# Optimization experiments

Measured on AMD Instinct MI355X. Metric: run time of the kernel, lower is better.

The kernel has to match this reference:

```python
import jax, jax.numpy as jnp
import numpy as np

N = 100_000       # nodes
E = 600_000       # edges
D_IN = 128
D_OUT = 128


def setup_inputs() -> dict:
    key = jax.random.key(0)
    k0, k1, k2, k3, k4, k5 = jax.random.split(key, 6)
    node_feature = jax.random.normal(k0, (N, D_IN), dtype=jnp.float32)
    edge_index = jax.random.randint(k1, (2, E), 0, N, dtype=jnp.int32)
    s = 1.0 / np.sqrt(D_IN)  # torch nn.Linear default init range
    W1 = jax.random.uniform(k2, (D_OUT, D_IN), jnp.float32, -s, s)
    b1 = jax.random.uniform(k3, (D_OUT,), jnp.float32, -s, s)
    W2 = jax.random.uniform(k4, (D_OUT, D_IN), jnp.float32, -s, s)
    b2 = jax.random.uniform(k5, (D_OUT,), jnp.float32, -s, s)
    return {"node_feature": node_feature, "edge_index": edge_index,
            "W1": W1, "b1": b1, "W2": W2, "b2": b2}


def reference(node_feature, edge_index, W1, b1, W2, b2):
    # h1 = lin1(x)
    h1 = node_feature @ W1.T + b1                       # [N, D_OUT]
    src, dst = edge_index[0], edge_index[1]
    # scatter(x[src], dst, reduce='mul', dim_size=N): segment product,
    # identity 1 for nodes with no incoming edges
    msgs = node_feature[src]                            # [E, D_IN]
    aggr = jax.ops.segment_prod(msgs, dst, num_segments=N)  # [N, D_IN]
    h2 = aggr @ W2.T + b2                               # [N, D_OUT]
    return h1 * h2
```

## Files before the change

### kernel.cpp

```cpp
#include <hip/hip_runtime.h>

#define NN 100000
#define NE 600000
#define D  128
#define CAP 64
#define NT (NN / 16)

typedef __attribute__((ext_vector_type(8))) short short8;
typedef __attribute__((ext_vector_type(4))) float floatx4;

__device__ __forceinline__ unsigned short f2bf(float f) {
    union { float f; unsigned int u; } a; a.f = f;
    unsigned int r = a.u + 0x7fff + ((a.u >> 16) & 1);
    return (unsigned short)(r >> 16);
}
__device__ __forceinline__ float bf2f(unsigned short h) {
    union { unsigned int u; float f; } a; a.u = ((unsigned int)h) << 16;
    return a.f;
}

__global__ __launch_bounds__(256) void prep_kernel(const float* __restrict__ W1,
                                                   const float* __restrict__ W2,
                                                   short8* __restrict__ wfrag,
                                                   int* __restrict__ counts) {
    int idx = blockIdx.x * 256 + threadIdx.x;
    for (int j = idx; j < NN; j += 4096) counts[j] = 0;

    int m2 = idx >> 11;
    int rem = idx & 2047;
    int c = rem >> 8;
    int q = (rem >> 6) & 3;
    int l = rem & 63;
    const float* W = m2 ? W2 : W1;
    int row = c * 16 + (l & 15);
    int kb = q * 32 + 8 * (l >> 4);
    const float* src = &W[row * D + kb];
    short8 h, lo;
#pragma unroll
    for (int j = 0; j < 8; ++j) {
        float v = src[j];
        unsigned short hh = f2bf(v);
        h[j]  = (short)hh;
        lo[j] = (short)f2bf(v - bf2f(hh));
    }
    wfrag[(((m2 * 2 + 0) * 8 + c) * 4 + q) * 64 + l] = h;
    wfrag[(((m2 * 2 + 1) * 8 + c) * 4 + q) * 64 + l] = lo;
}


__global__ void bucket_kernel(const int* __restrict__ src, const int* __restrict__ dst,
                              int* __restrict__ counts, int* __restrict__ bucket, int e) {
    int i = blockIdx.x * blockDim.x + threadIdx.x;
    if (i < e) {
        int d = dst[i];
        int pos = atomicAdd(&counts[d], 1);
        if (pos < CAP) bucket[(size_t)d * CAP + pos] = src[i];
    }
}

__global__ __launch_bounds__(512, 1)
void fused_kernel(const float* __restrict__ x,
                  const int* __restrict__ counts,
                  const int* __restrict__ bucket,
                  const short8* __restrict__ wfrag,
                  const float* __restrict__ b1,
                  const float* __restrict__ b2,
                  float* __restrict__ out) {
    __shared__ short8 sW[2 * 8 * 4 * 64];

    const int lane = threadIdx.x & 63;
    const int wv   = threadIdx.x >> 6;
    const int r16  = lane & 15;
    const int g    = lane >> 4;

    const int tile = blockIdx.x * 8 + wv;
    const bool live = (tile < NT);
    const int base = tile * 16;
    const size_t rowoff = live ? ((size_t)(base + r16) * D + g * 8) : 0;

    short8 st[8];
#pragma unroll
    for (int k = 0; k < 8; ++k) st[k] = wfrag[threadIdx.x + k * 512];

    floatx4 p[8];
#pragma unroll
    for (int k = 0; k < 8; ++k) p[k] = (floatx4)1.f;
    if (live) {
        const int node = base + r16;
        int cnt = counts[node]; if (cnt > CAP) cnt = CAP;
        const int* bp = &bucket[(size_t)node * CAP];
        int i = 0;
        for (; i + 2 <= cnt; i += 2) {
            int s0 = bp[i], s1 = bp[i + 1];
            const float* xr0 = &x[(size_t)s0 * D + g * 8];
            const float* xr1 = &x[(size_t)s1 * D + g * 8];
#pragma unroll
            for (int q = 0; q < 4; ++q) {
                floatx4 a0 = *(const floatx4*)&xr0[q * 32];
                floatx4 a1 = *(const floatx4*)&xr0[q * 32 + 4];
                floatx4 c0 = *(const floatx4*)&xr1[q * 32];
                floatx4 c1 = *(const floatx4*)&xr1[q * 32 + 4];
                p[2 * q]     *= a0 * c0;
                p[2 * q + 1] *= a1 * c1;
            }
        }
        if (i < cnt) {
            int s0 = bp[i];
            const float* xr0 = &x[(size_t)s0 * D + g * 8];
#pragma unroll
            for (int q = 0; q < 4; ++q) {
                p[2 * q]     *= *(const floatx4*)&xr0[q * 32];
                p[2 * q + 1] *= *(const floatx4*)&xr0[q * 32 + 4];
            }
        }
    }
    short8 gh[4], gl[4];
#pragma unroll
    for (int q = 0; q < 4; ++q) {
        short8 h, l;
#pragma unroll
        for (int jj = 0; jj < 4; ++jj) {
            unsigned short hh = f2bf(p[2 * q][jj]);
            h[jj] = (short)hh;
            l[jj] = (short)f2bf(p[2 * q][jj] - bf2f(hh));
            unsigned short hh2 = f2bf(p[2 * q + 1][jj]);
            h[4 + jj] = (short)hh2;
            l[4 + jj] = (short)f2bf(p[2 * q + 1][jj] - bf2f(hh2));
        }
        gh[q] = h; gl[q] = l;
    }

#pragma unroll
    for (int k = 0; k < 8; ++k) sW[threadIdx.x + k * 512] = st[k];
    __syncthreads();

    floatx4 acc[8];
#pragma unroll
    for (int c = 0; c < 8; ++c) acc[c] = (floatx4)0.f;

    floatx4 h1[8];
    if (live) {
        const float* xr = &x[rowoff];
#pragma unroll
        for (int q = 0; q < 4; ++q) {
            floatx4 v0 = *(const floatx4*)&xr[q * 32];
            floatx4 v1 = *(const floatx4*)&xr[q * 32 + 4];
            short8 fh, fl;
#pragma unroll
            for (int jj = 0; jj < 4; ++jj) {
                unsigned short hh = f2bf(v0[jj]);
                fh[jj] = (short)hh;
                fl[jj] = (short)f2bf(v0[jj] - bf2f(hh));
                unsigned short hh2 = f2bf(v1[jj]);
                fh[4 + jj] = (short)hh2;
                fl[4 + jj] = (short)f2bf(v1[jj] - bf2f(hh2));
            }
#pragma unroll
            for (int c = 0; c < 8; ++c) {
                short8 bh = sW[((0 * 8 + c) * 4 + q) * 64 + lane];
                short8 bl = sW[((1 * 8 + c) * 4 + q) * 64 + lane];
                acc[c] = __builtin_amdgcn_mfma_f32_16x16x32_bf16(fh, bh, acc[c], 0, 0, 0);
                acc[c] = __builtin_amdgcn_mfma_f32_16x16x32_bf16(fl, bh, acc[c], 0, 0, 0);
                acc[c] = __builtin_amdgcn_mfma_f32_16x16x32_bf16(fh, bl, acc[c], 0, 0, 0);
            }
        }
#pragma unroll
        for (int c = 0; c < 8; ++c) {
            float bb = b1[c * 16 + r16];
            floatx4 t = acc[c];
            t[0] += bb; t[1] += bb; t[2] += bb; t[3] += bb;
            h1[c] = t;
            acc[c] = (floatx4)0.f;
        }
    }

    __syncthreads();
    for (int i = threadIdx.x; i < 4096; i += 512) sW[i] = wfrag[4096 + i];
    __syncthreads();

    if (live) {
#pragma unroll
        for (int q = 0; q < 4; ++q) {
#pragma unroll
            for (int c = 0; c < 8; ++c) {
                short8 bh = sW[((0 * 8 + c) * 4 + q) * 64 + lane];
                short8 bl = sW[((1 * 8 + c) * 4 + q) * 64 + lane];
                acc[c] = __builtin_amdgcn_mfma_f32_16x16x32_bf16(gh[q], bh, acc[c], 0, 0, 0);
                acc[c] = __builtin_amdgcn_mfma_f32_16x16x32_bf16(gl[q], bh, acc[c], 0, 0, 0);
                acc[c] = __builtin_amdgcn_mfma_f32_16x16x32_bf16(gh[q], bl, acc[c], 0, 0, 0);
            }
        }
#pragma unroll
        for (int c = 0; c < 8; ++c) {
            float bb = b2[c * 16 + r16];
#pragma unroll
            for (int r = 0; r < 4; ++r) {
                out[(size_t)(base + g * 4 + r) * D + c * 16 + r16] =
                    h1[c][r] * (acc[c][r] + bb);
            }
        }
    }
}


extern "C" void kernel_launch(void* const* d_in, const int* in_sizes, int n_in,
                              void* d_out, int out_size, void* d_ws, size_t ws_size,
                              hipStream_t stream) {
    const float* x  = (const float*)d_in[0];
    const int*   ei = (const int*)d_in[1];
    const float* W1 = (const float*)d_in[2];
    const float* b1 = (const float*)d_in[3];
    const float* W2 = (const float*)d_in[4];
    const float* b2 = (const float*)d_in[5];
    float* out = (float*)d_out;

    const int n = NN, e = NE;
    const int* src = ei;
    const int* dst = ei + e;

    char* ws = (char*)d_ws;
    short8* wfrag = (short8*)ws;                ws += 8192 * 16;
    int* counts = (int*)ws;                     ws += (size_t)n * sizeof(int);
    ws += 256 - ((uintptr_t)ws & 255);
    int* bucket = (int*)ws;

    prep_kernel<<<16, 256, 0, stream>>>(W1, W2, wfrag, counts);
    bucket_kernel<<<(e + 255) / 256, 256, 0, stream>>>(src, dst, counts, bucket, e);
    fused_kernel<<<(NT + 7) / 8, 512, 0, stream>>>(x, counts, bucket, wfrag, b1, b2, out);
}
```

Before: 131.8 us.

## Sort nodes by in-degree so each wave gathers for similar-degree rows

Adds a degree histogram, a scan and a counting-sort permutation of nodes by clamped in-degree. The fused kernel then processes tiles of permuted nodes and scatters output rows through the permutation. This balances per-lane gather loop trip counts within a wave, reducing divergence from the max-degree lane. It adds three small kernels plus a memset, and makes x row reads and output writes non-contiguous.

```diff
diff --git a/kernel.cpp b/kernel.cpp
--- a/kernel.cpp
+++ b/kernel.cpp
@@ -21,11 +21,8 @@
 
 __global__ __launch_bounds__(256) void prep_kernel(const float* __restrict__ W1,
                                                    const float* __restrict__ W2,
-                                                   short8* __restrict__ wfrag,
-                                                   int* __restrict__ counts) {
+                                                   short8* __restrict__ wfrag) {
     int idx = blockIdx.x * 256 + threadIdx.x;
-    for (int j = idx; j < NN; j += 4096) counts[j] = 0;
-
     int m2 = idx >> 11;
     int rem = idx & 2047;
     int c = rem >> 8;
@@ -58,10 +55,59 @@
     }
 }
 
+
+__global__ __launch_bounds__(256) void dhist_kernel(const int* __restrict__ counts,
+                                                    int* __restrict__ dhist, int n) {
+    __shared__ int lh[CAP + 1];
+    int t = threadIdx.x;
+    if (t <= CAP) lh[t] = 0;
+    __syncthreads();
+    int i = blockIdx.x * 256 + t;
+    if (i < n) {
+        int d = counts[i]; if (d > CAP) d = CAP;
+        atomicAdd(&lh[d], 1);
+    }
+    __syncthreads();
+    if (t <= CAP && lh[t]) atomicAdd(&dhist[t], lh[t]);
+}
+
+
+__global__ __launch_bounds__(64) void dscan_kernel(const int* __restrict__ dhist,
+                                                   int* __restrict__ dcur) {
+    if (threadIdx.x == 0) {
+        int run = 0;
+        for (int d = 0; d <= CAP; ++d) { dcur[d] = run; run += dhist[d]; }
+    }
+}
+
+
+__global__ __launch_bounds__(256) void perm_kernel(const int* __restrict__ counts,
+                                                   int* __restrict__ dcur,
+                                                   int* __restrict__ perm, int n) {
+    __shared__ int lh[CAP + 1], lbase[CAP + 1], lcur[CAP + 1];
+    int t = threadIdx.x;
+    if (t <= CAP) { lh[t] = 0; lcur[t] = 0; }
+    __syncthreads();
+    int i = blockIdx.x * 256 + t;
+    int d = 0;
+    if (i < n) {
+        d = counts[i]; if (d > CAP) d = CAP;
+        atomicAdd(&lh[d], 1);
+    }
+    __syncthreads();
+    if (t <= CAP && lh[t]) lbase[t] = atomicAdd(&dcur[t], lh[t]);
+    __syncthreads();
+    if (i < n) {
+        int r = atomicAdd(&lcur[d], 1);
+        perm[lbase[d] + r] = i;
+    }
+}
+
 __global__ __launch_bounds__(512, 1)
 void fused_kernel(const float* __restrict__ x,
                   const int* __restrict__ counts,
                   const int* __restrict__ bucket,
+                  const int* __restrict__ perm,
                   const short8* __restrict__ wfrag,
                   const float* __restrict__ b1,
                   const float* __restrict__ b2,
@@ -76,19 +122,21 @@
     const int tile = blockIdx.x * 8 + wv;
     const bool live = (tile < NT);
     const int base = tile * 16;
-    const size_t rowoff = live ? ((size_t)(base + r16) * D + g * 8) : 0;
 
     short8 st[8];
 #pragma unroll
     for (int k = 0; k < 8; ++k) st[k] = wfrag[threadIdx.x + k * 512];
+
+    const int anode = live ? perm[base + r16] : 0;
+    int4 wrows = live ? *(const int4*)&perm[base + g * 4] : make_int4(0, 0, 0, 0);
+    const size_t rowoff = (size_t)anode * D + g * 8;
 
     floatx4 p[8];
 #pragma unroll
     for (int k = 0; k < 8; ++k) p[k] = (floatx4)1.f;
     if (live) {
-        const int node = base + r16;
-        int cnt = counts[node]; if (cnt > CAP) cnt = CAP;
-        const int* bp = &bucket[(size_t)node * CAP];
+        int cnt = counts[anode]; if (cnt > CAP) cnt = CAP;
+        const int* bp = &bucket[(size_t)anode * CAP];
         int i = 0;
         for (; i + 2 <= cnt; i += 2) {
             int s0 = bp[i], s1 = bp[i + 1];
@@ -190,12 +238,13 @@
                 acc[c] = __builtin_amdgcn_mfma_f32_16x16x32_bf16(gh[q], bl, acc[c], 0, 0, 0);
             }
         }
+        const int wr[4] = { wrows.x, wrows.y, wrows.z, wrows.w };
 #pragma unroll
         for (int c = 0; c < 8; ++c) {
             float bb = b2[c * 16 + r16];
 #pragma unroll
             for (int r = 0; r < 4; ++r) {
-                out[(size_t)(base + g * 4 + r) * D + c * 16 + r16] =
+                out[(size_t)wr[r] * D + c * 16 + r16] =
                     h1[c][r] * (acc[c][r] + bb);
             }
         }
@@ -221,10 +270,18 @@
     char* ws = (char*)d_ws;
     short8* wfrag = (short8*)ws;                ws += 8192 * 16;
     int* counts = (int*)ws;                     ws += (size_t)n * sizeof(int);
+    int* dhist = (int*)ws;                      ws += (CAP + 1) * sizeof(int);
+    int* dcur = (int*)ws;                       ws += (CAP + 1) * sizeof(int);
+    ws += 256 - ((uintptr_t)ws & 255);
+    int* perm = (int*)ws;                       ws += (size_t)n * sizeof(int);
     ws += 256 - ((uintptr_t)ws & 255);
     int* bucket = (int*)ws;
 
-    prep_kernel<<<16, 256, 0, stream>>>(W1, W2, wfrag, counts);
+    hipMemsetAsync(counts, 0, ((size_t)n + CAP + 1) * sizeof(int), stream);
+    prep_kernel<<<16, 256, 0, stream>>>(W1, W2, wfrag);
     bucket_kernel<<<(e + 255) / 256, 256, 0, stream>>>(src, dst, counts, bucket, e);
-    fused_kernel<<<(NT + 7) / 8, 512, 0, stream>>>(x, counts, bucket, wfrag, b1, b2, out);
-}
+    dhist_kernel<<<(n + 255) / 256, 256, 0, stream>>>(counts, dhist, n);
+    dscan_kernel<<<1, 64, 0, stream>>>(dhist, dcur);
+    perm_kernel<<<(n + 255) / 256, 256, 0, stream>>>(counts, dcur, perm, n);
+    fused_kernel<<<(NT + 7) / 8, 512, 0, stream>>>(x, counts, bucket, perm, wfrag, b1, b2, out);
+}
```

New measurement: 160.4 us. 1.22x slower.
